# Kernel optimization log

Measured on AMD Instinct MI355X. Metric: run time of the kernel, lower is better.

Reference implementation:

```python
import jax, jax.numpy as jnp
import numpy as np

NUM_HEADS = 6

def setup_inputs() -> dict:
    key = jax.random.key(0)
    k1, k2, k3 = jax.random.split(key, 3)
    B, N, C = 8, 4096, 768
    x = jax.random.normal(k1, (B, N, C), dtype=jnp.float32)
    # torch Linear weights, stored here as (in, out) so y = x @ w
    w_qkv = jax.random.normal(k2, (C, 3 * C), dtype=jnp.float32) * (C ** -0.5)
    w_proj = jax.random.normal(k3, (C, C), dtype=jnp.float32) * (C ** -0.5)
    b_proj = jnp.zeros((C,), dtype=jnp.float32)
    return {"x": x, "w_qkv": w_qkv, "w_proj": w_proj, "b_proj": b_proj}

def reference(x, w_qkv, w_proj, b_proj):
    B, N, C = x.shape
    H = NUM_HEADS
    D = C // H
    scale = D ** -0.5
    qkv = (x @ w_qkv).reshape(B, N, 3, H, D)
    q, k, v = qkv[:, :, 0], qkv[:, :, 1], qkv[:, :, 2]  # each (B, N, H, D)
    # NOTE: faithful to source — no permute, so attention is over the HEAD axis
    attn = jnp.einsum('bnhd,bngd->bnhg', q, k) * scale  # (B, N, H, H)
    attn = jax.nn.softmax(attn, axis=-1)
    out = jnp.einsum('bnhg,bngd->bnhd', attn, v)        # (B, N, H, D)
    # torch: .transpose(1,2).reshape(B, N, C) — replicate the exact dim mixing
    out = jnp.transpose(out, (0, 2, 1, 3)).reshape(B, N, C)
    return out @ w_proj + b_proj
```

## Files before the change

kernel.cpp:

```cpp
#include <hip/hip_runtime.h>
#include <hip/hip_bf16.h>
#include <stdint.h>

typedef __attribute__((ext_vector_type(8))) short short8;
typedef __attribute__((ext_vector_type(4))) float floatx4;

#define DEVINL static __device__ __forceinline__

DEVINL float bf2f(uint32_t u) {
  union { uint32_t i; float f; } x; x.i = u << 16; return x.f;
}
DEVINL float bfu(short v) {
  union { uint32_t i; float f; } x; x.i = ((uint32_t)(uint16_t)v) << 16; return x.f;
}
DEVINL uint16_t f2bf(float f) {
  union { float f; uint32_t i; } x; x.f = f;
  uint32_t i = x.i;
  i += 0x7fff + ((i >> 16) & 1);
  return (uint16_t)(i >> 16);
}

__global__ __launch_bounds__(256)
void k_cvt_bf16(const float* __restrict__ in, uint16_t* __restrict__ out, int n4) {
  int i = blockIdx.x * blockDim.x + threadIdx.x;
  int stride = gridDim.x * blockDim.x;
  for (; i < n4; i += stride) {
    float4 v = ((const float4*)in)[i];
    ushort4 o;
    o.x = f2bf(v.x); o.y = f2bf(v.y); o.z = f2bf(v.z); o.w = f2bf(v.w);
    ((ushort4*)out)[i] = o;
  }
}

__global__ __launch_bounds__(256)
void k_transpose_bf16(const float* __restrict__ in, uint16_t* __restrict__ out, int K, int N) {
  int idx = blockIdx.x * 256 + threadIdx.x;
  if (idx >= N * K) return;
  int n = idx / K;
  int k = idx - n * K;
  out[idx] = f2bf(in[(long)k * N + n]);
}

template<int OUT_BF16>
__global__ __launch_bounds__(512, 2)
void k_gemm256(const uint16_t* __restrict__ A,
               const uint16_t* __restrict__ B,
               void* __restrict__ Cout,
               const float* __restrict__ bias,
               int M, int N, int Kd, int tilesN)
{
  __shared__ uint16_t As[2][2][8192];
  __shared__ uint16_t Bs[2][2][8192];

  const int nwg = gridDim.x;
  const int orig = blockIdx.x;
  const int q = nwg >> 3, r = nwg & 7;
  const int xcd = orig & 7, seq = orig >> 3;
  const int wgid = (xcd < r ? xcd * (q + 1) : r * (q + 1) + (xcd - r) * q) + seq;
  const int mt = wgid / tilesN;
  const int nt = wgid - mt * tilesN;

  const int t = threadIdx.x;
  const int l = t & 63;
  const int w = t >> 6;
  const int wm = w >> 2;
  const int wn = w & 3;
  const long m0 = (long)mt * 256;
  const long n0 = (long)nt * 256;

  const int srow0 = t >> 3;
  const int scol  = ((l & 7) ^ (l >> 3)) * 8;
  const int wbyte = w * 1024;

  const uint16_t* Abase = A + m0 * Kd;
  const uint16_t* Bbase = B + n0 * Kd;

  const int fr = l & 15;
  const int kg = l >> 4;
  const int xorv = (l & 7) << 4;
  const int cb0 = (kg * 16) ^ xorv;
  const int cb1 = (64 + kg * 16) ^ xorv;

  floatx4 acc[8][4];
#pragma unroll
  for (int m = 0; m < 8; ++m)
#pragma unroll
    for (int n = 0; n < 4; ++n)
      acc[m][n] = (floatx4){0.f, 0.f, 0.f, 0.f};

  const int nK = Kd >> 6;

  auto stage = [&](uint16_t* ldsHalf, const uint16_t* gHalf, int ktile) {
    const uint16_t* g0 = gHalf + (long)srow0 * Kd + ktile * 64 + scol;
    __builtin_amdgcn_global_load_lds(
        (const __attribute__((address_space(1))) void*)g0,
        (__attribute__((address_space(3))) void*)((char*)ldsHalf + wbyte), 16, 0, 0);
    __builtin_amdgcn_global_load_lds(
        (const __attribute__((address_space(1))) void*)(g0 + (long)64 * Kd),
        (__attribute__((address_space(3))) void*)((char*)ldsHalf + 8192 + wbyte), 16, 0, 0);
  };
  auto rdA = [&](int buf, int mm, int kk) -> short8 {
    const char* p = (const char*)&As[buf][wm][0] + mm * 2048 + fr * 128 + (kk ? cb1 : cb0);
    return *(const short8*)p;
  };
  auto rdB = [&](int buf, int nn, int kk) -> short8 {
    const char* p = (const char*)&Bs[buf][wn >> 1][0] + (wn & 1) * 8192 + nn * 2048 + fr * 128
                    + (kk ? cb1 : cb0);
    return *(const short8*)p;
  };

  stage(&Bs[0][0][0], Bbase, 0);
  stage(&As[0][0][0], Abase, 0);
  stage(&Bs[0][1][0], Bbase + (long)128 * Kd, 0);
  stage(&As[0][1][0], Abase + (long)128 * Kd, 0);
  {
    int t1 = 1 % nK;
    stage(&Bs[t1 & 1][0][0], Bbase, t1);
    stage(&As[t1 & 1][0][0], Abase, t1);
  }
  asm volatile("s_waitcnt vmcnt(4)" ::: "memory");
  __builtin_amdgcn_s_barrier();

  short8 a[4][2], bv0[2][2], bv1[2][2];

  for (int kt = 0; kt < nK; ++kt) {
    const int cbuf = kt & 1;
    const int nbuf = cbuf ^ 1;
    const int t1 = (kt + 1) % nK;
    const int t2 = (kt + 2) % nK;

#pragma unroll
    for (int mm = 0; mm < 4; ++mm) { a[mm][0] = rdA(cbuf, mm, 0); a[mm][1] = rdA(cbuf, mm, 1); }
#pragma unroll
    for (int nn = 0; nn < 2; ++nn) { bv0[nn][0] = rdB(cbuf, nn, 0); bv0[nn][1] = rdB(cbuf, nn, 1); }
#pragma unroll
    for (int nn = 0; nn < 2; ++nn) { bv1[nn][0] = rdB(cbuf, 2 + nn, 0); bv1[nn][1] = rdB(cbuf, 2 + nn, 1); }
    stage(&Bs[nbuf][1][0], Bbase + (long)128 * Kd, t1);
    stage(&As[nbuf][1][0], Abase + (long)128 * Kd, t1);
    asm volatile("s_waitcnt lgkmcnt(8)" ::: "memory");
    __builtin_amdgcn_s_barrier();
    asm volatile("s_waitcnt lgkmcnt(0)" ::: "memory");
    __builtin_amdgcn_s_setprio(1);
#pragma unroll
    for (int mm = 0; mm < 4; ++mm)
#pragma unroll
      for (int nn = 0; nn < 2; ++nn) {
        acc[mm][nn] = __builtin_amdgcn_mfma_f32_16x16x32_bf16(a[mm][0], bv0[nn][0], acc[mm][nn], 0, 0, 0);
        acc[mm][nn] = __builtin_amdgcn_mfma_f32_16x16x32_bf16(a[mm][1], bv0[nn][1], acc[mm][nn], 0, 0, 0);
        acc[mm][2 + nn] = __builtin_amdgcn_mfma_f32_16x16x32_bf16(a[mm][0], bv1[nn][0], acc[mm][2 + nn], 0, 0, 0);
        acc[mm][2 + nn] = __builtin_amdgcn_mfma_f32_16x16x32_bf16(a[mm][1], bv1[nn][1], acc[mm][2 + nn], 0, 0, 0);
      }
    __builtin_amdgcn_s_setprio(0);
    __builtin_amdgcn_s_barrier();

#pragma unroll
    for (int mm = 0; mm < 4; ++mm) { a[mm][0] = rdA(cbuf, 4 + mm, 0); a[mm][1] = rdA(cbuf, 4 + mm, 1); }
    stage(&Bs[cbuf][0][0], Bbase, t2);
    asm volatile("s_waitcnt lgkmcnt(0)" ::: "memory");
    __builtin_amdgcn_s_barrier();
    stage(&As[cbuf][0][0], Abase, t2);
    asm volatile("s_waitcnt vmcnt(4)" ::: "memory");
    __builtin_amdgcn_s_setprio(1);
#pragma unroll
    for (int mm = 0; mm < 4; ++mm)
#pragma unroll
      for (int nn = 0; nn < 2; ++nn) {
        acc[4 + mm][2 + nn] = __builtin_amdgcn_mfma_f32_16x16x32_bf16(a[mm][0], bv1[nn][0], acc[4 + mm][2 + nn], 0, 0, 0);
        acc[4 + mm][2 + nn] = __builtin_amdgcn_mfma_f32_16x16x32_bf16(a[mm][1], bv1[nn][1], acc[4 + mm][2 + nn], 0, 0, 0);
        acc[4 + mm][nn] = __builtin_amdgcn_mfma_f32_16x16x32_bf16(a[mm][0], bv0[nn][0], acc[4 + mm][nn], 0, 0, 0);
        acc[4 + mm][nn] = __builtin_amdgcn_mfma_f32_16x16x32_bf16(a[mm][1], bv0[nn][1], acc[4 + mm][nn], 0, 0, 0);
      }
    __builtin_amdgcn_s_setprio(0);
    __builtin_amdgcn_s_barrier();
  }

  asm volatile("s_waitcnt vmcnt(0)" ::: "memory");
  __builtin_amdgcn_s_barrier();

  const int orow = (l >> 4) * 4;
  const int ocol = l & 15;
  if (OUT_BF16) {
    uint16_t* C = (uint16_t*)Cout;
    char* eb = (char*)&As[0][0][0] + (size_t)w * 4096;
    const int rr0 = l >> 3;
    const int cc0 = (l & 7) * 8;
#pragma unroll
    for (int mm = 0; mm < 8; ++mm) {
#pragma unroll
      for (int nn = 0; nn < 4; ++nn)
#pragma unroll
        for (int r2 = 0; r2 < 4; ++r2) {
          int rrow = orow + r2;
          int byo = ((rrow * 64 + nn * 16 + ocol) * 2) ^ ((rrow & 7) << 4);
          *(uint16_t*)(eb + byo) = f2bf(acc[mm][nn][r2]);
        }
#pragma unroll
      for (int p = 0; p < 2; ++p) {
        int rrow = rr0 + p * 8;
        int byo = ((rrow * 64 + cc0) * 2) ^ ((rrow & 7) << 4);
        short8 vvv = *(const short8*)(eb + byo);
        *(short8*)(&C[(m0 + wm * 128 + mm * 16 + rrow) * N + n0 + wn * 64 + cc0]) = vvv;
      }
    }
  } else {
    float* C = (float*)Cout;
    float* eb = (float*)&As[0][0][0] + (size_t)w * 1024;
    const int rr0 = l >> 4;
    const int cc0 = (l & 15) * 4;
    float4 bias4 = make_float4(0.f, 0.f, 0.f, 0.f);
    if (bias) bias4 = *(const float4*)(bias + n0 + wn * 64 + cc0);
#pragma unroll
    for (int mm = 0; mm < 8; ++mm) {
#pragma unroll
      for (int nn = 0; nn < 4; ++nn)
#pragma unroll
        for (int r2 = 0; r2 < 4; ++r2)
          eb[(orow + r2) * 64 + nn * 16 + ocol] = acc[mm][nn][r2];
#pragma unroll
      for (int p = 0; p < 4; ++p) {
        int rrow = rr0 + p * 4;
        float4 vvv = *(const float4*)(eb + rrow * 64 + cc0);
        vvv.x += bias4.x; vvv.y += bias4.y; vvv.z += bias4.z; vvv.w += bias4.w;
        *(float4*)(&C[(m0 + wm * 128 + mm * 16 + rrow) * N + n0 + wn * 64 + cc0]) = vvv;
      }
    }
  }
}

__global__ __launch_bounds__(256)
void k_attn(const uint16_t* __restrict__ qkv, uint16_t* __restrict__ outp) {
  const int wid = blockIdx.x * 4 + (threadIdx.x >> 6);
  const int l = threadIdx.x & 63;
  const int sub = l >> 4;
  const int i = l & 15;
  const int token = wid * 4 + sub;
  const uint16_t* row = qkv + (long)token * 2304 + i * 8;

  short8 kv[6];
  float qf[6][8];
#pragma unroll
  for (int h = 0; h < 6; ++h) {
    short8 qv = *(const short8*)(row + h * 128);
    kv[h] = *(const short8*)(row + 768 + h * 128);
#pragma unroll
    for (int e = 0; e < 8; ++e) qf[h][e] = bfu(qv[e]);
  }

  float s[36];
#pragma unroll
  for (int g = 0; g < 6; ++g) {
    float kf[8];
#pragma unroll
    for (int e = 0; e < 8; ++e) kf[e] = bfu(kv[g][e]);
#pragma unroll
    for (int h = 0; h < 6; ++h) {
      float a = 0.f;
#pragma unroll
      for (int e = 0; e < 8; ++e) a += qf[h][e] * kf[e];
      s[h * 6 + g] = a;
    }
  }

#pragma unroll
  for (int off = 8; off > 0; off >>= 1)
#pragma unroll
    for (int j = 0; j < 36; ++j)
      s[j] += __shfl_xor(s[j], off, 64);

  const float scale = 0.088388347648318447f;
  float p[36];
#pragma unroll
  for (int h = 0; h < 6; ++h) {
    float mx = s[h * 6];
#pragma unroll
    for (int g = 1; g < 6; ++g) mx = fmaxf(mx, s[h * 6 + g]);
    float sum = 0.f;
#pragma unroll
    for (int g = 0; g < 6; ++g) {
      float e = __expf((s[h * 6 + g] - mx) * scale);
      p[h * 6 + g] = e; sum += e;
    }
    float inv = 1.f / sum;
#pragma unroll
    for (int g = 0; g < 6; ++g) p[h * 6 + g] *= inv;
  }

  float o[6][8];
#pragma unroll
  for (int h = 0; h < 6; ++h)
#pragma unroll
    for (int e = 0; e < 8; ++e) o[h][e] = 0.f;
#pragma unroll
  for (int g = 0; g < 6; ++g) {
    short8 vv = *(const short8*)(row + 1536 + g * 128);
    float vf[8];
#pragma unroll
    for (int e = 0; e < 8; ++e) vf[e] = bfu(vv[e]);
#pragma unroll
    for (int h = 0; h < 6; ++h)
#pragma unroll
      for (int e = 0; e < 8; ++e) o[h][e] += p[h * 6 + g] * vf[e];
  }

  const int b = token >> 12, nn = token & 4095;
#pragma unroll
  for (int h = 0; h < 6; ++h) {
    short8 ov;
#pragma unroll
    for (int e = 0; e < 8; ++e) ov[e] = (short)f2bf(o[h][e]);
    *(short8*)(outp + ((long)(b * 6 + h) * 4096 + nn) * 128 + i * 8) = ov;
  }
}

extern "C" void kernel_launch(void* const* d_in, const int* in_sizes, int n_in,
                              void* d_out, int out_size, void* d_ws, size_t ws_size,
                              hipStream_t stream) {
  const float* x      = (const float*)d_in[0];
  const float* w_qkv  = (const float*)d_in[1];
  const float* w_proj = (const float*)d_in[2];
  const float* b_proj = (const float*)d_in[3];
  float* out = (float*)d_out;

  const int Cc = 768, C3 = 2304;
  const int Mtok = in_sizes[0] / Cc;

  char* ws = (char*)d_ws;
  uint16_t* x_bf   = (uint16_t*)ws;
  uint16_t* att_bf = x_bf;
  uint16_t* qkv_bf = (uint16_t*)(ws + 50331648);
  uint16_t* wqkvT  = (uint16_t*)(ws + 50331648 + 150994944);
  uint16_t* wprojT = (uint16_t*)(ws + 50331648 + 150994944 + 3538944);

  hipLaunchKernelGGL(k_cvt_bf16, dim3(2048), dim3(256), 0, stream,
                     x, x_bf, Mtok * Cc / 4);
  hipLaunchKernelGGL(k_transpose_bf16, dim3((C3 * Cc + 255) / 256), dim3(256), 0, stream,
                     w_qkv, wqkvT, Cc, C3);
  hipLaunchKernelGGL(k_transpose_bf16, dim3((Cc * Cc + 255) / 256), dim3(256), 0, stream,
                     w_proj, wprojT, Cc, Cc);

  hipLaunchKernelGGL((k_gemm256<1>), dim3((Mtok / 256) * (C3 / 256)), dim3(512), 0, stream,
                     x_bf, wqkvT, (void*)qkv_bf, (const float*)nullptr, Mtok, C3, Cc, C3 / 256);

  hipLaunchKernelGGL(k_attn, dim3(Mtok / 16), dim3(256), 0, stream, qkv_bf, att_bf);

  hipLaunchKernelGGL((k_gemm256<0>), dim3((Mtok / 256) * (Cc / 256)), dim3(512), 0, stream,
                     att_bf, wprojT, (void*)out, b_proj, Mtok, Cc, Cc, Cc / 256);
}
```

Baseline: 261.8 us.

## Tile weight transpose through LDS and simplify GEMM double-buffer pipeline

The weight transpose kernel now moves 64x64 tiles through padded shared memory, so both its global reads and writes are coalesced instead of strided. The GEMM main loop drops the interleaved half-tile staging: each iteration prefetches the whole next k-tile into the other buffer, reads both A halves up front, and ends with one vmcnt(0) wait and a barrier in place of several barriers. This means fewer barriers per iteration, but it gives up the deeper two-stage prefetch. Waiting for every outstanding load each iteration may expose global-load latency, and holding the extra a2 fragments raises register pressure.

Result: no change. 262.9 us (+0.4%).

```diff
diff --git a/kernel.cpp b/kernel.cpp
--- a/kernel.cpp
+++ b/kernel.cpp
@@ -34,11 +34,18 @@
 
 __global__ __launch_bounds__(256)
 void k_transpose_bf16(const float* __restrict__ in, uint16_t* __restrict__ out, int K, int N) {
-  int idx = blockIdx.x * 256 + threadIdx.x;
-  if (idx >= N * K) return;
-  int n = idx / K;
-  int k = idx - n * K;
-  out[idx] = f2bf(in[(long)k * N + n]);
+  __shared__ float tile[64][65];
+  const int tn = blockIdx.x * 64;
+  const int tk = blockIdx.y * 64;
+  const int tx = threadIdx.x & 63;
+  const int ty = threadIdx.x >> 6;
+#pragma unroll
+  for (int i = 0; i < 64; i += 4)
+    tile[ty + i][tx] = in[(long)(tk + ty + i) * N + tn + tx];
+  __syncthreads();
+#pragma unroll
+  for (int i = 0; i < 64; i += 4)
+    out[(long)(tn + ty + i) * K + tk + tx] = f2bf(tile[tx][ty + i]);
 }
 
 template<int OUT_BF16>
@@ -110,24 +117,17 @@
   };
 
   stage(&Bs[0][0][0], Bbase, 0);
+  stage(&Bs[0][1][0], Bbase + (long)128 * Kd, 0);
   stage(&As[0][0][0], Abase, 0);
-  stage(&Bs[0][1][0], Bbase + (long)128 * Kd, 0);
   stage(&As[0][1][0], Abase + (long)128 * Kd, 0);
-  {
-    int t1 = 1 % nK;
-    stage(&Bs[t1 & 1][0][0], Bbase, t1);
-    stage(&As[t1 & 1][0][0], Abase, t1);
-  }
-  asm volatile("s_waitcnt vmcnt(4)" ::: "memory");
+  asm volatile("s_waitcnt vmcnt(0)" ::: "memory");
   __builtin_amdgcn_s_barrier();
 
-  short8 a[4][2], bv0[2][2], bv1[2][2];
+  short8 a[4][2], a2[4][2], bv0[2][2], bv1[2][2];
 
   for (int kt = 0; kt < nK; ++kt) {
     const int cbuf = kt & 1;
     const int nbuf = cbuf ^ 1;
-    const int t1 = (kt + 1) % nK;
-    const int t2 = (kt + 2) % nK;
 
 #pragma unroll
     for (int mm = 0; mm < 4; ++mm) { a[mm][0] = rdA(cbuf, mm, 0); a[mm][1] = rdA(cbuf, mm, 1); }
@@ -135,11 +135,18 @@
     for (int nn = 0; nn < 2; ++nn) { bv0[nn][0] = rdB(cbuf, nn, 0); bv0[nn][1] = rdB(cbuf, nn, 1); }
 #pragma unroll
     for (int nn = 0; nn < 2; ++nn) { bv1[nn][0] = rdB(cbuf, 2 + nn, 0); bv1[nn][1] = rdB(cbuf, 2 + nn, 1); }
-    stage(&Bs[nbuf][1][0], Bbase + (long)128 * Kd, t1);
-    stage(&As[nbuf][1][0], Abase + (long)128 * Kd, t1);
+
+    if (kt + 1 < nK) {
+      stage(&Bs[nbuf][0][0], Bbase, kt + 1);
+      stage(&Bs[nbuf][1][0], Bbase + (long)128 * Kd, kt + 1);
+      stage(&As[nbuf][0][0], Abase, kt + 1);
+      stage(&As[nbuf][1][0], Abase + (long)128 * Kd, kt + 1);
+    }
+
+#pragma unroll
+    for (int mm = 0; mm < 4; ++mm) { a2[mm][0] = rdA(cbuf, 4 + mm, 0); a2[mm][1] = rdA(cbuf, 4 + mm, 1); }
+
     asm volatile("s_waitcnt lgkmcnt(8)" ::: "memory");
-    __builtin_amdgcn_s_barrier();
-    asm volatile("s_waitcnt lgkmcnt(0)" ::: "memory");
     __builtin_amdgcn_s_setprio(1);
 #pragma unroll
     for (int mm = 0; mm < 4; ++mm)
@@ -150,32 +157,21 @@
         acc[mm][2 + nn] = __builtin_amdgcn_mfma_f32_16x16x32_bf16(a[mm][0], bv1[nn][0], acc[mm][2 + nn], 0, 0, 0);
         acc[mm][2 + nn] = __builtin_amdgcn_mfma_f32_16x16x32_bf16(a[mm][1], bv1[nn][1], acc[mm][2 + nn], 0, 0, 0);
       }
-    __builtin_amdgcn_s_setprio(0);
-    __builtin_amdgcn_s_barrier();
-
-#pragma unroll
-    for (int mm = 0; mm < 4; ++mm) { a[mm][0] = rdA(cbuf, 4 + mm, 0); a[mm][1] = rdA(cbuf, 4 + mm, 1); }
-    stage(&Bs[cbuf][0][0], Bbase, t2);
     asm volatile("s_waitcnt lgkmcnt(0)" ::: "memory");
-    __builtin_amdgcn_s_barrier();
-    stage(&As[cbuf][0][0], Abase, t2);
-    asm volatile("s_waitcnt vmcnt(4)" ::: "memory");
-    __builtin_amdgcn_s_setprio(1);
 #pragma unroll
     for (int mm = 0; mm < 4; ++mm)
 #pragma unroll
       for (int nn = 0; nn < 2; ++nn) {
-        acc[4 + mm][2 + nn] = __builtin_amdgcn_mfma_f32_16x16x32_bf16(a[mm][0], bv1[nn][0], acc[4 + mm][2 + nn], 0, 0, 0);
-        acc[4 + mm][2 + nn] = __builtin_amdgcn_mfma_f32_16x16x32_bf16(a[mm][1], bv1[nn][1], acc[4 + mm][2 + nn], 0, 0, 0);
-        acc[4 + mm][nn] = __builtin_amdgcn_mfma_f32_16x16x32_bf16(a[mm][0], bv0[nn][0], acc[4 + mm][nn], 0, 0, 0);
-        acc[4 + mm][nn] = __builtin_amdgcn_mfma_f32_16x16x32_bf16(a[mm][1], bv0[nn][1], acc[4 + mm][nn], 0, 0, 0);
+        acc[4 + mm][nn] = __builtin_amdgcn_mfma_f32_16x16x32_bf16(a2[mm][0], bv0[nn][0], acc[4 + mm][nn], 0, 0, 0);
+        acc[4 + mm][nn] = __builtin_amdgcn_mfma_f32_16x16x32_bf16(a2[mm][1], bv0[nn][1], acc[4 + mm][nn], 0, 0, 0);
+        acc[4 + mm][2 + nn] = __builtin_amdgcn_mfma_f32_16x16x32_bf16(a2[mm][0], bv1[nn][0], acc[4 + mm][2 + nn], 0, 0, 0);
+        acc[4 + mm][2 + nn] = __builtin_amdgcn_mfma_f32_16x16x32_bf16(a2[mm][1], bv1[nn][1], acc[4 + mm][2 + nn], 0, 0, 0);
       }
     __builtin_amdgcn_s_setprio(0);
+
+    asm volatile("s_waitcnt vmcnt(0)" ::: "memory");
     __builtin_amdgcn_s_barrier();
   }
-
-  asm volatile("s_waitcnt vmcnt(0)" ::: "memory");
-  __builtin_amdgcn_s_barrier();
 
   const int orow = (l >> 4) * 4;
   const int ocol = l & 15;
@@ -333,9 +329,9 @@
 
   hipLaunchKernelGGL(k_cvt_bf16, dim3(2048), dim3(256), 0, stream,
                      x, x_bf, Mtok * Cc / 4);
-  hipLaunchKernelGGL(k_transpose_bf16, dim3((C3 * Cc + 255) / 256), dim3(256), 0, stream,
+  hipLaunchKernelGGL(k_transpose_bf16, dim3(C3 / 64, Cc / 64), dim3(256), 0, stream,
                      w_qkv, wqkvT, Cc, C3);
-  hipLaunchKernelGGL(k_transpose_bf16, dim3((Cc * Cc + 255) / 256), dim3(256), 0, stream,
+  hipLaunchKernelGGL(k_transpose_bf16, dim3(Cc / 64, Cc / 64), dim3(256), 0, stream,
                      w_proj, wprojT, Cc, Cc);
 
   hipLaunchKernelGGL((k_gemm256<1>), dim3((Mtok / 256) * (C3 / 256)), dim3(512), 0, stream,
```
